# Performance work log

Measured on AMD Instinct MI355X. Metric: run time of the kernel, lower is better.

Reference implementation:

```python
import jax, jax.numpy as jnp
import numpy as np

N_NODES = 50000
N_EDGES = 1600000
F_NODE = 8
F_EDGE = 4
HIDDEN = 16
OUT = 8
MLP_HID = 25


def _nnconv(x, src, dst, edge_attr, wa, ba, wb, bb, root, bias, out_ch):
    # edge MLP -> per-edge weight matrix [E, in_ch, out_ch]
    h = jax.nn.relu(edge_attr @ wa + ba) @ wb + bb
    w = h.reshape(-1, x.shape[1], out_ch)
    # gather source node feats, per-edge small matmul
    msg = jnp.einsum('ei,eio->eo', x[src], w)  # [E, out_ch]
    n = x.shape[0]
    agg = jax.ops.segment_sum(msg, dst, num_segments=n)
    cnt = jax.ops.segment_sum(jnp.ones((msg.shape[0],), msg.dtype), dst, num_segments=n)
    agg = agg / jnp.maximum(cnt, 1.0)[:, None]  # mean aggregation
    return agg + x @ root + bias  # root weight + bias (PyG NNConv defaults)


def setup_inputs() -> dict:
    key = jax.random.key(0)
    ks = jax.random.split(key, 16)
    s = lambda k, shape, fan: jax.random.normal(k, shape, jnp.float32) * (1.0 / np.sqrt(fan))
    return {
        'x': jax.random.normal(ks[0], (N_NODES, F_NODE), jnp.float32),
        'edge_index': jax.random.randint(ks[1], (2, N_EDGES), 0, N_NODES),
        'edge_attr': jax.random.normal(ks[2], (N_EDGES, F_EDGE), jnp.float32),
        # conv1 edge-MLP: F_EDGE -> 25 -> F_NODE*HIDDEN
        'w1a': s(ks[3], (F_EDGE, MLP_HID), F_EDGE), 'b1a': jnp.zeros((MLP_HID,), jnp.float32),
        'w1b': s(ks[4], (MLP_HID, F_NODE * HIDDEN), MLP_HID), 'b1b': jnp.zeros((F_NODE * HIDDEN,), jnp.float32),
        'root1': s(ks[5], (F_NODE, HIDDEN), F_NODE), 'bias1': jnp.zeros((HIDDEN,), jnp.float32),
        # conv2 edge-MLP: F_EDGE -> 25 -> HIDDEN*OUT
        'w2a': s(ks[6], (F_EDGE, MLP_HID), F_EDGE), 'b2a': jnp.zeros((MLP_HID,), jnp.float32),
        'w2b': s(ks[7], (MLP_HID, HIDDEN * OUT), MLP_HID), 'b2b': jnp.zeros((HIDDEN * OUT,), jnp.float32),
        'root2': s(ks[8], (HIDDEN, OUT), HIDDEN), 'bias2': jnp.zeros((OUT,), jnp.float32),
    }


def reference(x, edge_index, edge_attr, w1a, b1a, w1b, b1b, root1, bias1,
              w2a, b2a, w2b, b2b, root2, bias2):
    src, dst = edge_index[0], edge_index[1]
    h = _nnconv(x, src, dst, edge_attr, w1a, b1a, w1b, b1b, root1, bias1, HIDDEN)
    h = jax.nn.relu(h)
    # dropout p=0.5 is identity in eval mode
    out = _nnconv(h, src, dst, edge_attr, w2a, b2a, w2b, b2b, root2, bias2, OUT)
    return out
```

## Files before the change

kernel.cpp:

```cpp
#include <hip/hip_runtime.h>
#include <hip/hip_fp16.h>

#define NN 50000
#define NE 1600000
#define FN 8
#define FE 4
#define HID 16
#define OC 8
#define MH 25
#define CAP 80
#define BINS 196
#define BCAP 8960
#define TILE 4096


typedef int iv4 __attribute__((ext_vector_type(4)));
static __device__ __forceinline__ int4 ntload4(const int4* p) {
    iv4 v = __builtin_nontemporal_load(reinterpret_cast<const iv4*>(p));
    return make_int4(v.x, v.y, v.z, v.w);
}
static __device__ __forceinline__ unsigned pack2h(float lo, float hi) {
    return ((unsigned)__half_as_ushort(__float2half_rn(hi)) << 16)
         |  (unsigned)__half_as_ushort(__float2half_rn(lo));
}

#define FMAMIX_ELO(acc, u, b) \
    asm("v_fma_mix_f32 %0, %1, %2, %0 op_sel:[0,0,0] op_sel_hi:[1,0,0]" \
        : "+v"(acc) : "v"(u), "v"(b))
#define FMAMIX_EHI(acc, u, b) \
    asm("v_fma_mix_f32 %0, %1, %2, %0 op_sel:[1,0,0] op_sel_hi:[1,0,0]" \
        : "+v"(acc) : "v"(u), "v"(b))
#define PKFMA(acc, a16, b) \
    asm("v_pk_fma_f16 %0, %1, %2, %0 op_sel:[0,0,0] op_sel_hi:[0,1,1]" \
        : "+v"(acc) : "v"(a16), "v"(b))

static __device__ __forceinline__ void unpack2(unsigned u, float& lo, float& hi) {
    __half2 h; *reinterpret_cast<unsigned*>(&h) = u;
    float2 f = __half22float2(h);
    lo = f.x; hi = f.y;
}

__global__ void __launch_bounds__(256) xhalf_kernel(const float4* __restrict__ x4,
                                                    uint4* __restrict__ xh4) {
    int n = blockIdx.x * 256 + threadIdx.x;
    if (n < NN) {
        float4 a = x4[2 * n], b = x4[2 * n + 1];
        xh4[n] = make_uint4(pack2h(a.x, a.y), pack2h(a.z, a.w),
                            pack2h(b.x, b.y), pack2h(b.z, b.w));
    }
}

__global__ void __launch_bounds__(256) binA_kernel(
    const int* __restrict__ ei, const float* __restrict__ ea,
    unsigned* __restrict__ gcursor, int4* __restrict__ binbuf) {
    __shared__ unsigned hist[BINS], basei[BINS], run[BINS];
    for (int t = threadIdx.x; t < BINS; t += 256) { hist[t] = 0u; run[t] = 0u; }
    __syncthreads();
    const int bb = blockIdx.x * TILE;
    int dsts[16], srcs[16];
    bool actk[4];
#pragma unroll
    for (int k = 0; k < 4; ++k) {
        int e = bb + k * 1024 + threadIdx.x * 4;
        actk[k] = e < NE;
        int4 d = make_int4(0, 0, 0, 0), s = make_int4(0, 0, 0, 0);
        if (actk[k]) {
            d = *reinterpret_cast<const int4*>(ei + NE + e);
            s = *reinterpret_cast<const int4*>(ei + e);
        }
        dsts[4 * k]     = d.x; dsts[4 * k + 1] = d.y;
        dsts[4 * k + 2] = d.z; dsts[4 * k + 3] = d.w;
        srcs[4 * k]     = s.x; srcs[4 * k + 1] = s.y;
        srcs[4 * k + 2] = s.z; srcs[4 * k + 3] = s.w;
        if (actk[k]) {
            atomicAdd(&hist[d.x >> 8], 1u);
            atomicAdd(&hist[d.y >> 8], 1u);
            atomicAdd(&hist[d.z >> 8], 1u);
            atomicAdd(&hist[d.w >> 8], 1u);
        }
    }
    __syncthreads();
    for (int t = threadIdx.x; t < BINS; t += 256)
        basei[t] = hist[t] ? atomicAdd(&gcursor[t], hist[t]) : 0u;
    __syncthreads();
#pragma unroll
    for (int k = 0; k < 4; ++k) {
        if (!actk[k]) continue;
        int e = bb + k * 1024 + threadIdx.x * 4;
#pragma unroll
        for (int j = 0; j < 4; ++j) {
            float4 a = *reinterpret_cast<const float4*>(ea + 4ull * (e + j));
            unsigned u01 = pack2h(a.x, a.y);
            unsigned u23 = pack2h(a.z, a.w);
            int d = dsts[4 * k + j];
            int b = d >> 8;
            unsigned off = atomicAdd(&run[b], 1u);
            unsigned slot = basei[b] + off;
            if (slot < BCAP)
                binbuf[(size_t)b * BCAP + slot] =
                    make_int4(srcs[4 * k + j], d, (int)u01, (int)u23);
        }
    }
}

__global__ void __launch_bounds__(512) binB_kernel(
    const int4* __restrict__ binbuf, const unsigned* __restrict__ gcursor,
    unsigned* __restrict__ cursorF, int4* __restrict__ recs) {
    int b   = blockIdx.x >> 2;
    int sub = blockIdx.x & 3;
    unsigned cnt = gcursor[b];
    if (cnt > BCAP) cnt = BCAP;
    const int4* srcp = binbuf + (size_t)b * BCAP;
    for (unsigned i = threadIdx.x + sub * 512u; i < cnt; i += 2048u) {
        int4 r = ntload4(srcp + i);
        int dst = r.y;
        unsigned pos = atomicAdd(&cursorF[dst], 1u);
        if (pos < CAP)
            recs[(size_t)dst * CAP + pos] = make_int4(r.x, r.z, r.w, 0);
    }
}

__global__ void __launch_bounds__(512, 8) conv1_kernel(
    const float* __restrict__ x, const __half* __restrict__ xh,
    const int4* __restrict__ recs, const unsigned* __restrict__ cnts,
    const float* __restrict__ wa, const float* __restrict__ ba,
    const float* __restrict__ wb, const float* __restrict__ bb,
    const float* __restrict__ root, const float* __restrict__ bias,
    float* __restrict__ hn)
{
    __shared__ float s_wa[FE * MH];
    __shared__ float s_ba[MH];
    __shared__ float s_wb[26 * 129];
    __shared__ float s_root[FN * HID];
    __shared__ float s_bias[HID];
    __shared__ uint2 s_ea[8][2][33];
    __shared__ uint4 s_g[8][2][33];
    for (int t = threadIdx.x; t < FE * MH; t += 512) s_wa[t] = wa[t];
    for (int t = threadIdx.x; t < MH; t += 512) s_ba[t] = ba[t];
    for (int t = threadIdx.x; t < 26 * 128; t += 512) {
        int r = t >> 7, c = t & 127;
        s_wb[r * 129 + c] = (r < MH) ? wb[t] : bb[c];
    }
    for (int t = threadIdx.x; t < FN * HID; t += 512) s_root[t] = root[t];
    for (int t = threadIdx.x; t < HID; t += 512) s_bias[t] = bias[t];
    __syncthreads();

    const float4* x4 = reinterpret_cast<const float4*>(x);
    const int w    = threadIdx.x >> 6;
    const int lane = threadIdx.x & 63;
    const int half = lane >> 5;
    const int m    = lane & 31;
    const int n = blockIdx.x * 16 + 2 * w + half;
    const unsigned cnt = cnts[n];
    const unsigned lim = cnt < CAP ? cnt : (unsigned)CAP;
    const size_t base = (size_t)n * CAP;
    unsigned limA = __shfl(lim, 0, 64);
    unsigned limB = __shfl(lim, 32, 64);
    unsigned cmax = limA > limB ? limA : limB;

    float w0 = 0.f, w1 = 0.f, w2 = 0.f, w3 = 0.f, b0 = 0.f;
    if (m < MH) { w0 = s_wa[m]; w1 = s_wa[MH + m]; w2 = s_wa[2 * MH + m];
                  w3 = s_wa[3 * MH + m]; b0 = s_ba[m]; }
    else if (m == MH) b0 = 1.f;

    unsigned T2[4] = {0u, 0u, 0u, 0u};
    for (unsigned c = 0; c < cmax; c += 32) {
        if (c + (unsigned)m < lim) {
            int4 r = ntload4(&recs[base + c + m]);
            s_ea[w][half][m] = make_uint2((unsigned)r.y, (unsigned)r.z);
            s_g[w][half][m] = *reinterpret_cast<const uint4*>(xh + 8ull * r.x);
        }
        asm volatile("s_waitcnt lgkmcnt(0)" ::: "memory");
        unsigned hi = (c + 32 < lim) ? c + 32 : lim;
        for (unsigned p = c; p < hi; ++p) {
            int j = p - c;
            uint2 eu = s_ea[w][half][j];
            uint4 gu = s_g[w][half][j];
            float hm = b0;
            FMAMIX_ELO(hm, eu.x, w0);
            FMAMIX_EHI(hm, eu.x, w1);
            FMAMIX_ELO(hm, eu.y, w2);
            FMAMIX_EHI(hm, eu.y, w3);
            hm = fmaxf(hm, 0.f);
            unsigned hm16 = (unsigned)__half_as_ushort(__float2half_rn(hm));
            PKFMA(T2[0], hm16, gu.x);
            PKFMA(T2[1], hm16, gu.y);
            PKFMA(T2[2], hm16, gu.z);
            PKFMA(T2[3], hm16, gu.w);
        }
        asm volatile("" ::: "memory");
    }

    float T[8];
    unpack2(T2[0], T[0], T[1]);
    unpack2(T2[1], T[2], T[3]);
    unpack2(T2[2], T[4], T[5]);
    unpack2(T2[3], T[6], T[7]);

    float s[16];
#pragma unroll
    for (int o = 0; o < 16; ++o) {
        float pm = 0.f;
        if (m < 26) {
            const float* wv = s_wb + m * 129 + o;
            pm = T[0]*wv[0]  + T[1]*wv[16] + T[2]*wv[32] + T[3]*wv[48]
               + T[4]*wv[64] + T[5]*wv[80] + T[6]*wv[96] + T[7]*wv[112];
        }
        pm += __shfl_xor(pm, 16, 32);
        pm += __shfl_xor(pm, 8, 32);
        pm += __shfl_xor(pm, 4, 32);
        pm += __shfl_xor(pm, 2, 32);
        pm += __shfl_xor(pm, 1, 32);
        s[o] = pm;
    }

    if (m == 0) {
        float inv = 1.f / fmaxf((float)cnt, 1.f);
        float4 xa = x4[2 * n], xb = x4[2 * n + 1];
        float xn[8] = {xa.x, xa.y, xa.z, xa.w, xb.x, xb.y, xb.z, xb.w};
        float v[16];
#pragma unroll
        for (int o = 0; o < 16; ++o) {
            float r = s[o] * inv + s_bias[o];
#pragma unroll
            for (int i = 0; i < 8; ++i) r += xn[i] * s_root[i * HID + o];
            v[o] = fmaxf(r, 0.f);
        }
        float4* hp = reinterpret_cast<float4*>(hn + 16ull * n);
        hp[0] = make_float4(v[0], v[1], v[2], v[3]);
        hp[1] = make_float4(v[4], v[5], v[6], v[7]);
        hp[2] = make_float4(v[8], v[9], v[10], v[11]);
        hp[3] = make_float4(v[12], v[13], v[14], v[15]);
    }
}

__global__ void __launch_bounds__(256) hn2h_kernel(const float4* __restrict__ hn4,
                                                   uint4* __restrict__ hh4) {
    int n = blockIdx.x * 256 + threadIdx.x;
    if (n < NN) {
        float4 a = hn4[4 * n],     b = hn4[4 * n + 1];
        float4 c = hn4[4 * n + 2], d = hn4[4 * n + 3];
        hh4[2 * n]     = make_uint4(pack2h(a.x, a.y), pack2h(a.z, a.w),
                                    pack2h(b.x, b.y), pack2h(b.z, b.w));
        hh4[2 * n + 1] = make_uint4(pack2h(c.x, c.y), pack2h(c.z, c.w),
                                    pack2h(d.x, d.y), pack2h(d.z, d.w));
    }
}

__global__ void __launch_bounds__(512, 8) conv2_kernel(
    const __half* __restrict__ hh, const int4* __restrict__ recs,
    const unsigned* __restrict__ cnts,
    const float* __restrict__ wa, const float* __restrict__ ba,
    const float* __restrict__ wb, const float* __restrict__ bb,
    const float* __restrict__ root, const float* __restrict__ bias,
    float* __restrict__ out)
{
    __shared__ float s_wa[FE * MH];
    __shared__ float s_ba[MH];
    __shared__ float s_wb[26 * 129];
    __shared__ float s_root[HID * OC];
    __shared__ float s_bias[OC];
    __shared__ uint2 s_ea[8][2][33];
    __shared__ uint4 s_gA[8][2][33];
    __shared__ uint4 s_gB[8][2][33];
    for (int t = threadIdx.x; t < FE * MH; t += 512) s_wa[t] = wa[t];
    for (int t = threadIdx.x; t < MH; t += 512) s_ba[t] = ba[t];
    for (int t = threadIdx.x; t < 26 * 128; t += 512) {
        int r = t >> 7, c = t & 127;
        s_wb[r * 129 + c] = (r < MH) ? wb[t] : bb[c];
    }
    for (int t = threadIdx.x; t < HID * OC; t += 512) s_root[t] = root[t];
    for (int t = threadIdx.x; t < OC; t += 512) s_bias[t] = bias[t];
    __syncthreads();

    const int w    = threadIdx.x >> 6;
    const int lane = threadIdx.x & 63;
    const int half = lane >> 5;
    const int m    = lane & 31;
    const int n = blockIdx.x * 16 + 2 * w + half;
    const unsigned cnt = cnts[n];
    const unsigned lim = cnt < CAP ? cnt : (unsigned)CAP;
    const size_t base = (size_t)n * CAP;
    unsigned limA = __shfl(lim, 0, 64);
    unsigned limB = __shfl(lim, 32, 64);
    unsigned cmax = limA > limB ? limA : limB;

    float w0 = 0.f, w1 = 0.f, w2 = 0.f, w3 = 0.f, b0 = 0.f;
    if (m < MH) { w0 = s_wa[m]; w1 = s_wa[MH + m]; w2 = s_wa[2 * MH + m];
                  w3 = s_wa[3 * MH + m]; b0 = s_ba[m]; }
    else if (m == MH) b0 = 1.f;

    unsigned T2[8] = {0u,0u,0u,0u,0u,0u,0u,0u};
    for (unsigned c = 0; c < cmax; c += 32) {
        if (c + (unsigned)m < lim) {
            int4 r = ntload4(&recs[base + c + m]);
            s_ea[w][half][m] = make_uint2((unsigned)r.y, (unsigned)r.z);
            const uint4* gp = reinterpret_cast<const uint4*>(hh + 16ull * r.x);
            s_gA[w][half][m] = gp[0];
            s_gB[w][half][m] = gp[1];
        }
        asm volatile("s_waitcnt lgkmcnt(0)" ::: "memory");
        unsigned hi = (c + 32 < lim) ? c + 32 : lim;
        for (unsigned p = c; p < hi; ++p) {
            int j = p - c;
            uint2 eu = s_ea[w][half][j];
            uint4 ga = s_gA[w][half][j];
            uint4 gb = s_gB[w][half][j];
            float hm = b0;
            FMAMIX_ELO(hm, eu.x, w0);
            FMAMIX_EHI(hm, eu.x, w1);
            FMAMIX_ELO(hm, eu.y, w2);
            FMAMIX_EHI(hm, eu.y, w3);
            hm = fmaxf(hm, 0.f);
            unsigned hm16 = (unsigned)__half_as_ushort(__float2half_rn(hm));
            PKFMA(T2[0], hm16, ga.x);
            PKFMA(T2[1], hm16, ga.y);
            PKFMA(T2[2], hm16, ga.z);
            PKFMA(T2[3], hm16, ga.w);
            PKFMA(T2[4], hm16, gb.x);
            PKFMA(T2[5], hm16, gb.y);
            PKFMA(T2[6], hm16, gb.z);
            PKFMA(T2[7], hm16, gb.w);
        }
        asm volatile("" ::: "memory");
    }

    float T[16];
#pragma unroll
    for (int i = 0; i < 8; ++i) unpack2(T2[i], T[2 * i], T[2 * i + 1]);

    float s[8];
#pragma unroll
    for (int o = 0; o < 8; ++o) {
        float pm = 0.f;
        if (m < 26) {
            const float* wv = s_wb + m * 129 + o;
            pm = T[0]*wv[0]   + T[1]*wv[8]   + T[2]*wv[16]  + T[3]*wv[24]
               + T[4]*wv[32]  + T[5]*wv[40]  + T[6]*wv[48]  + T[7]*wv[56]
               + T[8]*wv[64]  + T[9]*wv[72]  + T[10]*wv[80] + T[11]*wv[88]
               + T[12]*wv[96] + T[13]*wv[104]+ T[14]*wv[112]+ T[15]*wv[120];
        }
        pm += __shfl_xor(pm, 16, 32);
        pm += __shfl_xor(pm, 8, 32);
        pm += __shfl_xor(pm, 4, 32);
        pm += __shfl_xor(pm, 2, 32);
        pm += __shfl_xor(pm, 1, 32);
        s[o] = pm;
    }

    if (m == 0) {
        float inv = 1.f / fmaxf((float)cnt, 1.f);
        uint4 ha4 = *reinterpret_cast<const uint4*>(hh + 16ull * n);
        uint4 hb4 = *reinterpret_cast<const uint4*>(hh + 16ull * n + 8);
        const __half2* ap = reinterpret_cast<const __half2*>(&ha4);
        const __half2* bp = reinterpret_cast<const __half2*>(&hb4);
        float hnn[16];
#pragma unroll
        for (int i = 0; i < 4; ++i) {
            float2 fa = __half22float2(ap[i]);
            float2 fb = __half22float2(bp[i]);
            hnn[2 * i] = fa.x; hnn[2 * i + 1] = fa.y;
            hnn[8 + 2 * i] = fb.x; hnn[8 + 2 * i + 1] = fb.y;
        }
        float v[8];
#pragma unroll
        for (int o = 0; o < 8; ++o) {
            float r = s[o] * inv + s_bias[o];
#pragma unroll
            for (int i = 0; i < 16; ++i) r += hnn[i] * s_root[i * OC + o];
            v[o] = r;
        }
        float4* op = reinterpret_cast<float4*>(out + 8ull * n);
        op[0] = make_float4(v[0], v[1], v[2], v[3]);
        op[1] = make_float4(v[4], v[5], v[6], v[7]);
    }
}

extern "C" void kernel_launch(void* const* d_in, const int* in_sizes, int n_in,
                              void* d_out, int out_size, void* d_ws, size_t ws_size,
                              hipStream_t stream) {
    const float* x     = (const float*)d_in[0];
    const int*   ei    = (const int*)d_in[1];
    const float* ea    = (const float*)d_in[2];
    const float* w1a   = (const float*)d_in[3];
    const float* b1a   = (const float*)d_in[4];
    const float* w1b   = (const float*)d_in[5];
    const float* b1b   = (const float*)d_in[6];
    const float* root1 = (const float*)d_in[7];
    const float* bias1 = (const float*)d_in[8];
    const float* w2a   = (const float*)d_in[9];
    const float* b2a   = (const float*)d_in[10];
    const float* w2b   = (const float*)d_in[11];
    const float* b2b   = (const float*)d_in[12];
    const float* root2 = (const float*)d_in[13];
    const float* bias2 = (const float*)d_in[14];
    float* out = (float*)d_out;

    char* ws = (char*)d_ws;
    int4*     recs    = (int4*)(ws);
    unsigned* cursorF = (unsigned*)(ws + 64000000);
    unsigned* gcursor = (unsigned*)(ws + 64200000);
    float*    hn      = (float*)(ws + 64200800);
    __half*   hnh     = (__half*)(ws + 67400800);
    __half*   xh      = (__half*)(ws + 69000800);
    int4*     binbuf  = (int4*)(ws + 69800800);

    hipMemsetAsync(ws + 64000000, 0, 200784, stream);
    xhalf_kernel<<<(NN + 255) / 256, 256, 0, stream>>>((const float4*)x, (uint4*)xh);
    binA_kernel<<<(NE + TILE - 1) / TILE, 256, 0, stream>>>(ei, ea, gcursor, binbuf);
    binB_kernel<<<BINS * 4, 512, 0, stream>>>(binbuf, gcursor, cursorF, recs);
    conv1_kernel<<<NN / 16, 512, 0, stream>>>(x, xh, recs, cursorF,
                                              w1a, b1a, w1b, b1b, root1, bias1, hn);
    hn2h_kernel<<<(NN + 255) / 256, 256, 0, stream>>>((const float4*)hn, (uint4*)hnh);
    conv2_kernel<<<NN / 16, 512, 0, stream>>>(hnh, recs, cursorF,
                                              w2a, b2a, w2b, b2b, root2, bias2, out);
}
```

Before: 208.3 us.

## Map four nodes per wavefront with 16 lanes each handling two hidden units

The conv kernels now give each node 16 lanes instead of 32, and each lane computes two edge-MLP hidden units (m and m+16). That lets one 64-wide wavefront process four destination nodes. The edge loop always runs 16 unrolled iterations with an activity mask rather than a variable trip count, and the shared staging buffers are zeroed first so masked entries stay finite. This removes the lanes that sat idle on hidden units 26-31 and halves the number of blocks, at the cost of more registers per lane and wasted work on padded edges when node degrees within a wavefront differ.

```diff
diff --git a/kernel.cpp b/kernel.cpp
--- a/kernel.cpp
+++ b/kernel.cpp
@@ -133,8 +133,8 @@
     __shared__ float s_wb[26 * 129];
     __shared__ float s_root[FN * HID];
     __shared__ float s_bias[HID];
-    __shared__ uint2 s_ea[8][2][33];
-    __shared__ uint4 s_g[8][2][33];
+    __shared__ uint2 s_ea[8][4][17];
+    __shared__ uint4 s_g[8][4][17];
     for (int t = threadIdx.x; t < FE * MH; t += 512) s_wa[t] = wa[t];
     for (int t = threadIdx.x; t < MH; t += 512) s_ba[t] = ba[t];
     for (int t = threadIdx.x; t < 26 * 128; t += 512) {
@@ -143,78 +143,88 @@
     }
     for (int t = threadIdx.x; t < FN * HID; t += 512) s_root[t] = root[t];
     for (int t = threadIdx.x; t < HID; t += 512) s_bias[t] = bias[t];
+    {
+        float* pg = reinterpret_cast<float*>(&s_g[0][0][0]);
+        for (int t = threadIdx.x; t < 8 * 4 * 17 * 4; t += 512) pg[t] = 0.f;
+    }
     __syncthreads();
 
     const float4* x4 = reinterpret_cast<const float4*>(x);
-    const int w    = threadIdx.x >> 6;
-    const int lane = threadIdx.x & 63;
-    const int half = lane >> 5;
-    const int m    = lane & 31;
-    const int n = blockIdx.x * 16 + 2 * w + half;
-    const unsigned cnt = cnts[n];
+    const int w = threadIdx.x >> 6;
+    const int l = threadIdx.x & 63;
+    const int q = l >> 4;
+    const int m = l & 15;
+    const int n = blockIdx.x * 32 + w * 4 + q;
+    const unsigned cnt = (n < NN) ? cnts[n] : 0u;
     const unsigned lim = cnt < CAP ? cnt : (unsigned)CAP;
     const size_t base = (size_t)n * CAP;
-    unsigned limA = __shfl(lim, 0, 64);
-    unsigned limB = __shfl(lim, 32, 64);
-    unsigned cmax = limA > limB ? limA : limB;
-
-    float w0 = 0.f, w1 = 0.f, w2 = 0.f, w3 = 0.f, b0 = 0.f;
-    if (m < MH) { w0 = s_wa[m]; w1 = s_wa[MH + m]; w2 = s_wa[2 * MH + m];
-                  w3 = s_wa[3 * MH + m]; b0 = s_ba[m]; }
-    else if (m == MH) b0 = 1.f;
-
-    unsigned T2[4] = {0u, 0u, 0u, 0u};
-    for (unsigned c = 0; c < cmax; c += 32) {
+    unsigned cm = lim;
+    cm = max(cm, (unsigned)__shfl_xor((int)cm, 16));
+    cm = max(cm, (unsigned)__shfl_xor((int)cm, 32));
+
+    float w0a = s_wa[m], w1a = s_wa[MH + m], w2a = s_wa[2 * MH + m],
+          w3a = s_wa[3 * MH + m], b0a = s_ba[m];
+    const int m2 = m + 16;
+    float w0b = 0.f, w1b = 0.f, w2b = 0.f, w3b = 0.f, b0b = 0.f;
+    if (m2 < MH) { w0b = s_wa[m2]; w1b = s_wa[MH + m2]; w2b = s_wa[2 * MH + m2];
+                   w3b = s_wa[3 * MH + m2]; b0b = s_ba[m2]; }
+    else if (m2 == MH) b0b = 1.f;
+
+    unsigned TA[4] = {0u,0u,0u,0u}, TB[4] = {0u,0u,0u,0u};
+    for (unsigned c = 0; c < cm; c += 16) {
         if (c + (unsigned)m < lim) {
             int4 r = ntload4(&recs[base + c + m]);
-            s_ea[w][half][m] = make_uint2((unsigned)r.y, (unsigned)r.z);
-            s_g[w][half][m] = *reinterpret_cast<const uint4*>(xh + 8ull * r.x);
+            s_ea[w][q][m] = make_uint2((unsigned)r.y, (unsigned)r.z);
+            s_g[w][q][m] = *reinterpret_cast<const uint4*>(xh + 8ull * r.x);
         }
         asm volatile("s_waitcnt lgkmcnt(0)" ::: "memory");
-        unsigned hi = (c + 32 < lim) ? c + 32 : lim;
-        for (unsigned p = c; p < hi; ++p) {
-            int j = p - c;
-            uint2 eu = s_ea[w][half][j];
-            uint4 gu = s_g[w][half][j];
-            float hm = b0;
-            FMAMIX_ELO(hm, eu.x, w0);
-            FMAMIX_EHI(hm, eu.x, w1);
-            FMAMIX_ELO(hm, eu.y, w2);
-            FMAMIX_EHI(hm, eu.y, w3);
-            hm = fmaxf(hm, 0.f);
-            unsigned hm16 = (unsigned)__half_as_ushort(__float2half_rn(hm));
-            PKFMA(T2[0], hm16, gu.x);
-            PKFMA(T2[1], hm16, gu.y);
-            PKFMA(T2[2], hm16, gu.z);
-            PKFMA(T2[3], hm16, gu.w);
+#pragma unroll 4
+        for (int j = 0; j < 16; ++j) {
+            uint2 eu = s_ea[w][q][j];
+            uint4 gu = s_g[w][q][j];
+            float hmA = b0a, hmB = b0b;
+            FMAMIX_ELO(hmA, eu.x, w0a); FMAMIX_EHI(hmA, eu.x, w1a);
+            FMAMIX_ELO(hmA, eu.y, w2a); FMAMIX_EHI(hmA, eu.y, w3a);
+            FMAMIX_ELO(hmB, eu.x, w0b); FMAMIX_EHI(hmB, eu.x, w1b);
+            FMAMIX_ELO(hmB, eu.y, w2b); FMAMIX_EHI(hmB, eu.y, w3b);
+            hmA = fmaxf(hmA, 0.f); hmB = fmaxf(hmB, 0.f);
+            bool act = (c + (unsigned)j) < lim;
+            hmA = act ? hmA : 0.f;
+            hmB = act ? hmB : 0.f;
+            unsigned a16 = (unsigned)__half_as_ushort(__float2half_rn(hmA));
+            unsigned b16 = (unsigned)__half_as_ushort(__float2half_rn(hmB));
+            PKFMA(TA[0], a16, gu.x); PKFMA(TA[1], a16, gu.y);
+            PKFMA(TA[2], a16, gu.z); PKFMA(TA[3], a16, gu.w);
+            PKFMA(TB[0], b16, gu.x); PKFMA(TB[1], b16, gu.y);
+            PKFMA(TB[2], b16, gu.z); PKFMA(TB[3], b16, gu.w);
         }
         asm volatile("" ::: "memory");
     }
 
-    float T[8];
-    unpack2(T2[0], T[0], T[1]);
-    unpack2(T2[1], T[2], T[3]);
-    unpack2(T2[2], T[4], T[5]);
-    unpack2(T2[3], T[6], T[7]);
-
+    float T[8], U[8];
+    unpack2(TA[0], T[0], T[1]); unpack2(TA[1], T[2], T[3]);
+    unpack2(TA[2], T[4], T[5]); unpack2(TA[3], T[6], T[7]);
+    unpack2(TB[0], U[0], U[1]); unpack2(TB[1], U[2], U[3]);
+    unpack2(TB[2], U[4], U[5]); unpack2(TB[3], U[6], U[7]);
+
+    const int rb = (m2 <= MH) ? m2 : MH;
     float s[16];
 #pragma unroll
     for (int o = 0; o < 16; ++o) {
-        float pm = 0.f;
-        if (m < 26) {
-            const float* wv = s_wb + m * 129 + o;
-            pm = T[0]*wv[0]  + T[1]*wv[16] + T[2]*wv[32] + T[3]*wv[48]
-               + T[4]*wv[64] + T[5]*wv[80] + T[6]*wv[96] + T[7]*wv[112];
-        }
-        pm += __shfl_xor(pm, 16, 32);
-        pm += __shfl_xor(pm, 8, 32);
-        pm += __shfl_xor(pm, 4, 32);
-        pm += __shfl_xor(pm, 2, 32);
-        pm += __shfl_xor(pm, 1, 32);
+        const float* wv = s_wb + m * 129 + o;
+        const float* wu = s_wb + rb * 129 + o;
+        float pm = T[0]*wv[0]  + T[1]*wv[16] + T[2]*wv[32] + T[3]*wv[48]
+                 + T[4]*wv[64] + T[5]*wv[80] + T[6]*wv[96] + T[7]*wv[112]
+                 + U[0]*wu[0]  + U[1]*wu[16] + U[2]*wu[32] + U[3]*wu[48]
+                 + U[4]*wu[64] + U[5]*wu[80] + U[6]*wu[96] + U[7]*wu[112];
+        pm += __shfl_xor(pm, 8, 16);
+        pm += __shfl_xor(pm, 4, 16);
+        pm += __shfl_xor(pm, 2, 16);
+        pm += __shfl_xor(pm, 1, 16);
         s[o] = pm;
     }
 
-    if (m == 0) {
+    if (m == 0 && n < NN) {
         float inv = 1.f / fmaxf((float)cnt, 1.f);
         float4 xa = x4[2 * n], xb = x4[2 * n + 1];
         float xn[8] = {xa.x, xa.y, xa.z, xa.w, xb.x, xb.y, xb.z, xb.w};
@@ -260,9 +270,9 @@
     __shared__ float s_wb[26 * 129];
     __shared__ float s_root[HID * OC];
     __shared__ float s_bias[OC];
-    __shared__ uint2 s_ea[8][2][33];
-    __shared__ uint4 s_gA[8][2][33];
-    __shared__ uint4 s_gB[8][2][33];
+    __shared__ uint2 s_ea[8][4][17];
+    __shared__ uint4 s_gA[8][4][17];
+    __shared__ uint4 s_gB[8][4][17];
     for (int t = threadIdx.x; t < FE * MH; t += 512) s_wa[t] = wa[t];
     for (int t = threadIdx.x; t < MH; t += 512) s_ba[t] = ba[t];
     for (int t = threadIdx.x; t < 26 * 128; t += 512) {
@@ -271,84 +281,99 @@
     }
     for (int t = threadIdx.x; t < HID * OC; t += 512) s_root[t] = root[t];
     for (int t = threadIdx.x; t < OC; t += 512) s_bias[t] = bias[t];
+    {
+        float* pg = reinterpret_cast<float*>(&s_gA[0][0][0]);
+        for (int t = threadIdx.x; t < 8 * 4 * 17 * 4; t += 512) pg[t] = 0.f;
+        float* ph = reinterpret_cast<float*>(&s_gB[0][0][0]);
+        for (int t = threadIdx.x; t < 8 * 4 * 17 * 4; t += 512) ph[t] = 0.f;
+    }
     __syncthreads();
 
-    const int w    = threadIdx.x >> 6;
-    const int lane = threadIdx.x & 63;
-    const int half = lane >> 5;
-    const int m    = lane & 31;
-    const int n = blockIdx.x * 16 + 2 * w + half;
-    const unsigned cnt = cnts[n];
+    const int w = threadIdx.x >> 6;
+    const int l = threadIdx.x & 63;
+    const int q = l >> 4;
+    const int m = l & 15;
+    const int n = blockIdx.x * 32 + w * 4 + q;
+    const unsigned cnt = (n < NN) ? cnts[n] : 0u;
     const unsigned lim = cnt < CAP ? cnt : (unsigned)CAP;
     const size_t base = (size_t)n * CAP;
-    unsigned limA = __shfl(lim, 0, 64);
-    unsigned limB = __shfl(lim, 32, 64);
-    unsigned cmax = limA > limB ? limA : limB;
-
-    float w0 = 0.f, w1 = 0.f, w2 = 0.f, w3 = 0.f, b0 = 0.f;
-    if (m < MH) { w0 = s_wa[m]; w1 = s_wa[MH + m]; w2 = s_wa[2 * MH + m];
-                  w3 = s_wa[3 * MH + m]; b0 = s_ba[m]; }
-    else if (m == MH) b0 = 1.f;
-
-    unsigned T2[8] = {0u,0u,0u,0u,0u,0u,0u,0u};
-    for (unsigned c = 0; c < cmax; c += 32) {
+    unsigned cm = lim;
+    cm = max(cm, (unsigned)__shfl_xor((int)cm, 16));
+    cm = max(cm, (unsigned)__shfl_xor((int)cm, 32));
+
+    float w0a = s_wa[m], w1a = s_wa[MH + m], w2a = s_wa[2 * MH + m],
+          w3a = s_wa[3 * MH + m], b0a = s_ba[m];
+    const int m2 = m + 16;
+    float w0b = 0.f, w1b = 0.f, w2b = 0.f, w3b = 0.f, b0b = 0.f;
+    if (m2 < MH) { w0b = s_wa[m2]; w1b = s_wa[MH + m2]; w2b = s_wa[2 * MH + m2];
+                   w3b = s_wa[3 * MH + m2]; b0b = s_ba[m2]; }
+    else if (m2 == MH) b0b = 1.f;
+
+    unsigned TA[8] = {0u,0u,0u,0u,0u,0u,0u,0u};
+    unsigned TB[8] = {0u,0u,0u,0u,0u,0u,0u,0u};
+    for (unsigned c = 0; c < cm; c += 16) {
         if (c + (unsigned)m < lim) {
             int4 r = ntload4(&recs[base + c + m]);
-            s_ea[w][half][m] = make_uint2((unsigned)r.y, (unsigned)r.z);
+            s_ea[w][q][m] = make_uint2((unsigned)r.y, (unsigned)r.z);
             const uint4* gp = reinterpret_cast<const uint4*>(hh + 16ull * r.x);
-            s_gA[w][half][m] = gp[0];
-            s_gB[w][half][m] = gp[1];
+            s_gA[w][q][m] = gp[0];
+            s_gB[w][q][m] = gp[1];
         }
         asm volatile("s_waitcnt lgkmcnt(0)" ::: "memory");
-        unsigned hi = (c + 32 < lim) ? c + 32 : lim;
-        for (unsigned p = c; p < hi; ++p) {
-            int j = p - c;
-            uint2 eu = s_ea[w][half][j];
-            uint4 ga = s_gA[w][half][j];
-            uint4 gb = s_gB[w][half][j];
-            float hm = b0;
-            FMAMIX_ELO(hm, eu.x, w0);
-            FMAMIX_EHI(hm, eu.x, w1);
-            FMAMIX_ELO(hm, eu.y, w2);
-            FMAMIX_EHI(hm, eu.y, w3);
-            hm = fmaxf(hm, 0.f);
-            unsigned hm16 = (unsigned)__half_as_ushort(__float2half_rn(hm));
-            PKFMA(T2[0], hm16, ga.x);
-            PKFMA(T2[1], hm16, ga.y);
-            PKFMA(T2[2], hm16, ga.z);
-            PKFMA(T2[3], hm16, ga.w);
-            PKFMA(T2[4], hm16, gb.x);
-            PKFMA(T2[5], hm16, gb.y);
-            PKFMA(T2[6], hm16, gb.z);
-            PKFMA(T2[7], hm16, gb.w);
+#pragma unroll 4
+        for (int j = 0; j < 16; ++j) {
+            uint2 eu = s_ea[w][q][j];
+            uint4 ga = s_gA[w][q][j];
+            uint4 gb = s_gB[w][q][j];
+            float hmA = b0a, hmB = b0b;
+            FMAMIX_ELO(hmA, eu.x, w0a); FMAMIX_EHI(hmA, eu.x, w1a);
+            FMAMIX_ELO(hmA, eu.y, w2a); FMAMIX_EHI(hmA, eu.y, w3a);
+            FMAMIX_ELO(hmB, eu.x, w0b); FMAMIX_EHI(hmB, eu.x, w1b);
+            FMAMIX_ELO(hmB, eu.y, w2b); FMAMIX_EHI(hmB, eu.y, w3b);
+            hmA = fmaxf(hmA, 0.f); hmB = fmaxf(hmB, 0.f);
+            bool act = (c + (unsigned)j) < lim;
+            hmA = act ? hmA : 0.f;
+            hmB = act ? hmB : 0.f;
+            unsigned a16 = (unsigned)__half_as_ushort(__float2half_rn(hmA));
+            unsigned b16 = (unsigned)__half_as_ushort(__float2half_rn(hmB));
+            PKFMA(TA[0], a16, ga.x); PKFMA(TA[1], a16, ga.y);
+            PKFMA(TA[2], a16, ga.z); PKFMA(TA[3], a16, ga.w);
+            PKFMA(TA[4], a16, gb.x); PKFMA(TA[5], a16, gb.y);
+            PKFMA(TA[6], a16, gb.z); PKFMA(TA[7], a16, gb.w);
+            PKFMA(TB[0], b16, ga.x); PKFMA(TB[1], b16, ga.y);
+            PKFMA(TB[2], b16, ga.z); PKFMA(TB[3], b16, ga.w);
+            PKFMA(TB[4], b16, gb.x); PKFMA(TB[5], b16, gb.y);
+            PKFMA(TB[6], b16, gb.z); PKFMA(TB[7], b16, gb.w);
         }
         asm volatile("" ::: "memory");
     }
 
-    float T[16];
-#pragma unroll
-    for (int i = 0; i < 8; ++i) unpack2(T2[i], T[2 * i], T[2 * i + 1]);
-
+    float T[16], U[16];
+#pragma unroll
+    for (int i = 0; i < 8; ++i) {
+        unpack2(TA[i], T[2 * i], T[2 * i + 1]);
+        unpack2(TB[i], U[2 * i], U[2 * i + 1]);
+    }
+
+    const int rb = (m2 <= MH) ? m2 : MH;
     float s[8];
 #pragma unroll
     for (int o = 0; o < 8; ++o) {
+        const float* wv = s_wb + m * 129 + o;
+        const float* wu = s_wb + rb * 129 + o;
         float pm = 0.f;
-        if (m < 26) {
-            const float* wv = s_wb + m * 129 + o;
-            pm = T[0]*wv[0]   + T[1]*wv[8]   + T[2]*wv[16]  + T[3]*wv[24]
-               + T[4]*wv[32]  + T[5]*wv[40]  + T[6]*wv[48]  + T[7]*wv[56]
-               + T[8]*wv[64]  + T[9]*wv[72]  + T[10]*wv[80] + T[11]*wv[88]
-               + T[12]*wv[96] + T[13]*wv[104]+ T[14]*wv[112]+ T[15]*wv[120];
-        }
-        pm += __shfl_xor(pm, 16, 32);
-        pm += __shfl_xor(pm, 8, 32);
-        pm += __shfl_xor(pm, 4, 32);
-        pm += __shfl_xor(pm, 2, 32);
-        pm += __shfl_xor(pm, 1, 32);
+#pragma unroll
+        for (int i = 0; i < 16; ++i) pm += T[i] * wv[i * 8];
+#pragma unroll
+        for (int i = 0; i < 16; ++i) pm += U[i] * wu[i * 8];
+        pm += __shfl_xor(pm, 8, 16);
+        pm += __shfl_xor(pm, 4, 16);
+        pm += __shfl_xor(pm, 2, 16);
+        pm += __shfl_xor(pm, 1, 16);
         s[o] = pm;
     }
 
-    if (m == 0) {
+    if (m == 0 && n < NN) {
         float inv = 1.f / fmaxf((float)cnt, 1.f);
         uint4 ha4 = *reinterpret_cast<const uint4*>(hh + 16ull * n);
         uint4 hb4 = *reinterpret_cast<const uint4*>(hh + 16ull * n + 8);
@@ -409,9 +434,9 @@
     xhalf_kernel<<<(NN + 255) / 256, 256, 0, stream>>>((const float4*)x, (uint4*)xh);
     binA_kernel<<<(NE + TILE - 1) / TILE, 256, 0, stream>>>(ei, ea, gcursor, binbuf);
     binB_kernel<<<BINS * 4, 512, 0, stream>>>(binbuf, gcursor, cursorF, recs);
-    conv1_kernel<<<NN / 16, 512, 0, stream>>>(x, xh, recs, cursorF,
-                                              w1a, b1a, w1b, b1b, root1, bias1, hn);
+    conv1_kernel<<<(NN + 31) / 32, 512, 0, stream>>>(x, xh, recs, cursorF,
+                                                     w1a, b1a, w1b, b1b, root1, bias1, hn);
     hn2h_kernel<<<(NN + 255) / 256, 256, 0, stream>>>((const float4*)hn, (uint4*)hnh);
-    conv2_kernel<<<NN / 16, 512, 0, stream>>>(hnh, recs, cursorF,
-                                              w2a, b2a, w2b, b2b, root2, bias2, out);
-}
+    conv2_kernel<<<(NN + 31) / 32, 512, 0, stream>>>(hnh, recs, cursorF,
+                                                     w2a, b2a, w2b, b2b, root2, bias2, out);
+}
```

Result: faster. 198.4 us (-4.8%).
